# Kernel optimization log

Hardware: AMD Instinct MI355X
Metric: run time of the kernel (lower is better)

## Reference

```python
import jax, jax.numpy as jnp
import numpy as np

CH_IN = 256
CA = CH_IN // 8   # attention channels (theta/phi)
CH = CH_IN // 2   # value channels (g)


def _maxpool2(t):
    # 2x2 max pool, stride 2: (B,C,H,W) -> (B,C,H//2,W//2)
    b, c, h, w = t.shape
    return t.reshape(b, c, h // 2, 2, w // 2, 2).max(axis=(3, 5))


def setup_inputs() -> dict:
    key = jax.random.key(0)
    ks = jax.random.split(key, 6)
    B, H, W = 16, 64, 64
    x = jax.random.normal(ks[0], (B, CH_IN, H, W), dtype=jnp.float32)
    # 1x1 conv weights stored as (out_ch, in_ch); spectral_norm is a weight
    # reparameterization, so the forward math is a plain conv with these weights.
    s = 0.05
    w_theta = jax.random.normal(ks[1], (CA, CH_IN), dtype=jnp.float32) * s
    w_phi = jax.random.normal(ks[2], (CA, CH_IN), dtype=jnp.float32) * s
    w_g = jax.random.normal(ks[3], (CH, CH_IN), dtype=jnp.float32) * s
    w_o = jax.random.normal(ks[4], (CH_IN, CH), dtype=jnp.float32) * s
    # gamma is initialized to 0 in the module; use a nonzero value so the
    # attention branch contributes to the output.
    gamma = jnp.asarray(0.5, dtype=jnp.float32)
    return {"x": x, "w_theta": w_theta, "w_phi": w_phi, "w_g": w_g,
            "w_o": w_o, "gamma": gamma}


def reference(x, w_theta, w_phi, w_g, w_o, gamma):
    B, C, H, W = x.shape
    # 1x1 convs as channel contractions
    theta = jnp.einsum('oc,bchw->bohw', w_theta, x)            # (B,CA,H,W)
    phi = _maxpool2(jnp.einsum('oc,bchw->bohw', w_phi, x))     # (B,CA,H/2,W/2)
    g = _maxpool2(jnp.einsum('oc,bchw->bohw', w_g, x))         # (B,CH,H/2,W/2)
    N = H * W
    M = N // 4
    theta = theta.reshape(B, CA, N)
    phi = phi.reshape(B, CA, M)
    g = g.reshape(B, CH, M)
    # beta = softmax(theta^T phi) over keys (no scaling, as in original)
    beta = jax.nn.softmax(jnp.einsum('bcn,bcm->bnm', theta, phi), axis=-1)  # (B,N,M)
    o = jnp.einsum('bcm,bnm->bcn', g, beta).reshape(B, CH, H, W)
    o = jnp.einsum('oc,bchw->bohw', w_o, o)                    # (B,C,H,W)
    return gamma * o + x
```

## Files before the change

### kernel.cpp

```cpp
#include <hip/hip_runtime.h>
#include <hip/hip_bf16.h>

#define NB 16
#define CIN 256
#define CA 32
#define CH 128
#define NN 4096
#define MM 1024

typedef __attribute__((ext_vector_type(8))) short s16x8;
typedef __attribute__((ext_vector_type(4))) float f32x4;

static __device__ __forceinline__ unsigned short f2bf(float x) {
  __hip_bfloat16 h = __float2bfloat16(x);
  return __builtin_bit_cast(unsigned short, h);
}
static __device__ __forceinline__ float bf2f(unsigned short u) {
  unsigned int v = ((unsigned int)u) << 16;
  return __builtin_bit_cast(float, v);
}
static __device__ __forceinline__ void gload_lds16(const void* g, void* s) {
  __builtin_amdgcn_global_load_lds(
      (const __attribute__((address_space(1))) unsigned int*)g,
      (__attribute__((address_space(3))) unsigned int*)s, 16, 0, 0);
}

__global__ __launch_bounds__(256) void k_wcvt(const float* __restrict__ w_theta,
                                              const float* __restrict__ w_phi,
                                              const float* __restrict__ w_g,
                                              const float* __restrict__ w_o,
                                              unsigned short* __restrict__ wcat2,
                                              unsigned short* __restrict__ wo2) {
  const int i = blockIdx.x * 256 + threadIdx.x;
  if (i < 49152) {
    const int row = i >> 8, c = i & 255;
    const float v = (row < 32) ? w_theta[i]
                  : (row < 64) ? w_phi[i - 8192]
                               : w_g[i - 16384];
    const int dst = ((row >> 4) * 8 + (c >> 5)) * 512 +
                    (((c >> 3) & 3) * 16 + (row & 15)) * 8 + (c & 7);
    wcat2[dst] = f2bf(v);
  } else {
    const int w = i - 49152;
    const int c_out = w >> 7, k = w & 127;
    const int dst = (((c_out >> 4) * 16) + ((k >> 5) * 4) + ((k >> 3) & 3)) * 128 +
                    ((c_out & 15) << 3) + (k & 7);
    wo2[dst] = f2bf(w_o[w]);
  }
}

__global__ __launch_bounds__(512) void k_proj(const float* __restrict__ x,
                                              const unsigned short* __restrict__ wcat2,
                                              unsigned short* __restrict__ theta,
                                              unsigned short* __restrict__ phi2,
                                              unsigned short* __restrict__ g2) {
  __shared__ unsigned short xl[32][140];
  __shared__ unsigned short ol[192][136];
  const int b = blockIdx.y;
  const int t = blockIdx.x;
  const int tid = threadIdx.x;
  const int wv = tid >> 6;
  const int l = tid & 63;
  const int grp = l >> 4, col = l & 15;
  const float* xb = x + (size_t)b * CIN * NN;
  f32x4 acc[12];
#pragma unroll
  for (int r = 0; r < 12; ++r) acc[r] = f32x4{0.f, 0.f, 0.f, 0.f};
#pragma unroll 1
  for (int kc = 0; kc < 8; ++kc) {
#pragma unroll
    for (int s = 0; s < 2; ++s) {
      const int i = tid + s * 512;
      const int cl = i >> 5, nq = i & 31;
      const float4 v = *reinterpret_cast<const float4*>(
          xb + (size_t)(kc * 32 + cl) * NN + t * 128 + nq * 4);
      const unsigned int lo = (unsigned)f2bf(v.x) | ((unsigned)f2bf(v.y) << 16);
      const unsigned int hi = (unsigned)f2bf(v.z) | ((unsigned)f2bf(v.w) << 16);
      *reinterpret_cast<uint2*>(&xl[cl][nq * 4]) = make_uint2(lo, hi);
    }
    __syncthreads();
    s16x8 bfrag;
#pragma unroll
    for (int j = 0; j < 8; ++j)
      bfrag[j] = (short)xl[grp * 8 + j][wv * 16 + col];
#pragma unroll
    for (int r = 0; r < 12; ++r) {
      const s16x8 af = *reinterpret_cast<const s16x8*>(
          wcat2 + (size_t)(r * 8 + kc) * 512 + l * 8);
      acc[r] = __builtin_amdgcn_mfma_f32_16x16x32_bf16(af, bfrag, acc[r], 0, 0, 0);
    }
    __syncthreads();
  }
#pragma unroll
  for (int r = 0; r < 12; ++r)
#pragma unroll
    for (int q = 0; q < 4; ++q)
      ol[r * 16 + grp * 4 + q][wv * 16 + col] = f2bf(acc[r][q]);
  __syncthreads();
  unsigned short* thb = theta + (size_t)b * NN * CA;
  for (int i = tid; i < 128 * 16; i += 512) {
    const int n = i >> 4, cp = (i & 15) << 1;
    const unsigned int v = (unsigned)ol[cp][n] | ((unsigned)ol[cp + 1][n] << 16);
    *reinterpret_cast<unsigned int*>(thb + (size_t)(t * 128 + n) * CA + cp) = v;
  }
  unsigned short* phb2 = phi2 + (size_t)b * MM * CA;
  for (int i = tid; i < 32 * 32; i += 512) {
    const int ca = i & 31, mx = i >> 5;
    const float v = fmaxf(
        fmaxf(bf2f(ol[32 + ca][2 * mx]), bf2f(ol[32 + ca][2 * mx + 1])),
        fmaxf(bf2f(ol[32 + ca][64 + 2 * mx]), bf2f(ol[32 + ca][64 + 2 * mx + 1])));
    const int m = t * 32 + mx;
    phb2[(m >> 4) * 512 + (ca >> 3) * 128 + (m & 15) * 8 + (ca & 7)] = f2bf(v);
  }
  unsigned short* gb2 = g2 + (size_t)b * CH * MM;
  for (int i = tid; i < 128 * 32; i += 512) {
    const int mx = i & 31, c = i >> 5;
    const float v = fmaxf(
        fmaxf(bf2f(ol[64 + c][2 * mx]), bf2f(ol[64 + c][2 * mx + 1])),
        fmaxf(bf2f(ol[64 + c][64 + 2 * mx]), bf2f(ol[64 + c][64 + 2 * mx + 1])));
    gb2[(size_t)(t * 8 + (c >> 4)) * 512 + ((mx >> 3) & 3) * 128 + (c & 15) * 8 +
        (mx & 7)] = f2bf(v);
  }
}

__global__ __launch_bounds__(256, 3) void k_attn_out(
    const unsigned short* __restrict__ theta, const unsigned short* __restrict__ phi2,
    const unsigned short* __restrict__ g2, const unsigned short* __restrict__ wo2,
    const float* __restrict__ x, const float* __restrict__ gammap,
    float* __restrict__ out) {
  __shared__ __align__(16) unsigned short kv[2][10240];
  __shared__ __align__(16) unsigned short pl[4][16][72];
  const int b = blockIdx.y;
  const int tid = threadIdx.x;
  const int wv = tid >> 6;
  const int l = tid & 63;
  const int grp = l >> 4, col = l & 15;
  const int n0 = blockIdx.x * 128 + wv * 32;
  const unsigned short* thb = theta + (size_t)b * NN * CA;
  const unsigned short* ph2b = phi2 + (size_t)b * MM * CA;
  const unsigned short* gb2 = g2 + (size_t)b * CH * MM;
  const s16x8 qf0 = *reinterpret_cast<const s16x8*>(thb + (size_t)(n0 + col) * CA + grp * 8);
  const s16x8 qf1 = *reinterpret_cast<const s16x8*>(thb + (size_t)(n0 + 16 + col) * CA + grp * 8);

  auto STAGE = [&](int buf, int tile) {
    const int mc = tile * 64;
    const unsigned short* ksrc = ph2b + (mc >> 4) * 512;
    const unsigned short* vsrc = gb2 + (size_t)(mc >> 5) * 4096;
#pragma unroll
    for (int q = 0; q < 5; ++q) {
      const int i = wv * 5 + q;
      const unsigned short* src = (i < 4) ? (ksrc + i * 512) : (vsrc + (i - 4) * 512);
      gload_lds16(src + (size_t)l * 8, &kv[buf][i * 512]);
    }
  };

  f32x4 oa0[8], oa1[8];
#pragma unroll
  for (int t = 0; t < 8; ++t) {
    oa0[t] = f32x4{0.f, 0.f, 0.f, 0.f};
    oa1[t] = f32x4{0.f, 0.f, 0.f, 0.f};
  }
  float m0 = -INFINITY, l0 = 0.f, m1 = -INFINITY, l1 = 0.f;
  const f32x4 z4 = {0.f, 0.f, 0.f, 0.f};

  STAGE(0, 0);
  __syncthreads();
#pragma unroll 1
  for (int it = 0; it < 16; ++it) {
    const int cur = it & 1;
    if (it < 15) STAGE(cur ^ 1, it + 1);
    const unsigned short* kb = &kv[cur][0];
    const unsigned short* vb = &kv[cur][2048];
    const int fo = grp * 128 + col * 8;
    const s16x8 kf0 = *reinterpret_cast<const s16x8*>(kb + 0 * 512 + fo);
    const s16x8 kf1 = *reinterpret_cast<const s16x8*>(kb + 1 * 512 + fo);
    const s16x8 kf2 = *reinterpret_cast<const s16x8*>(kb + 2 * 512 + fo);
    const s16x8 kf3 = *reinterpret_cast<const s16x8*>(kb + 3 * 512 + fo);
    f32x4 s00 = __builtin_amdgcn_mfma_f32_16x16x32_bf16(kf0, qf0, z4, 0, 0, 0);
    f32x4 s01 = __builtin_amdgcn_mfma_f32_16x16x32_bf16(kf1, qf0, z4, 0, 0, 0);
    f32x4 s02 = __builtin_amdgcn_mfma_f32_16x16x32_bf16(kf2, qf0, z4, 0, 0, 0);
    f32x4 s03 = __builtin_amdgcn_mfma_f32_16x16x32_bf16(kf3, qf0, z4, 0, 0, 0);
    f32x4 s10 = __builtin_amdgcn_mfma_f32_16x16x32_bf16(kf0, qf1, z4, 0, 0, 0);
    f32x4 s11 = __builtin_amdgcn_mfma_f32_16x16x32_bf16(kf1, qf1, z4, 0, 0, 0);
    f32x4 s12 = __builtin_amdgcn_mfma_f32_16x16x32_bf16(kf2, qf1, z4, 0, 0, 0);
    f32x4 s13 = __builtin_amdgcn_mfma_f32_16x16x32_bf16(kf3, qf1, z4, 0, 0, 0);
    float cm0 = -INFINITY, cm1 = -INFINITY;
#pragma unroll
    for (int r = 0; r < 4; ++r) {
      cm0 = fmaxf(cm0, fmaxf(fmaxf(s00[r], s01[r]), fmaxf(s02[r], s03[r])));
      cm1 = fmaxf(cm1, fmaxf(fmaxf(s10[r], s11[r]), fmaxf(s12[r], s13[r])));
    }
    cm0 = fmaxf(cm0, __shfl_xor(cm0, 16));
    cm0 = fmaxf(cm0, __shfl_xor(cm0, 32));
    cm1 = fmaxf(cm1, __shfl_xor(cm1, 16));
    cm1 = fmaxf(cm1, __shfl_xor(cm1, 32));
    if (!__all(cm0 <= m0 + 8.f && cm1 <= m1 + 8.f)) {
      const float mn0 = fmaxf(m0, cm0), mn1 = fmaxf(m1, cm1);
      const float sc0 = __expf(m0 - mn0), sc1 = __expf(m1 - mn1);
      l0 *= sc0;
      l1 *= sc1;
#pragma unroll
      for (int t = 0; t < 8; ++t) {
#pragma unroll
        for (int r = 0; r < 4; ++r) {
          oa0[t][r] *= sc0;
          oa1[t][r] *= sc1;
        }
      }
      m0 = mn0;
      m1 = mn1;
    }
    s16x8 pfA0, pfB0, pfA1, pfB1;
    {
      float p0[4], p1[4], p2[4], p3[4];
      float cs = 0.f;
#pragma unroll
      for (int r = 0; r < 4; ++r) {
        p0[r] = __expf(s00[r] - m0);
        p1[r] = __expf(s01[r] - m0);
        p2[r] = __expf(s02[r] - m0);
        p3[r] = __expf(s03[r] - m0);
        cs += (p0[r] + p1[r]) + (p2[r] + p3[r]);
      }
      cs += __shfl_xor(cs, 16);
      cs += __shfl_xor(cs, 32);
      l0 += cs;
      *reinterpret_cast<uint2*>(&pl[wv][col][grp * 4]) =
          make_uint2((unsigned)f2bf(p0[0]) | ((unsigned)f2bf(p0[1]) << 16),
                     (unsigned)f2bf(p0[2]) | ((unsigned)f2bf(p0[3]) << 16));
      *reinterpret_cast<uint2*>(&pl[wv][col][16 + grp * 4]) =
          make_uint2((unsigned)f2bf(p1[0]) | ((unsigned)f2bf(p1[1]) << 16),
                     (unsigned)f2bf(p1[2]) | ((unsigned)f2bf(p1[3]) << 16));
      *reinterpret_cast<uint2*>(&pl[wv][col][32 + grp * 4]) =
          make_uint2((unsigned)f2bf(p2[0]) | ((unsigned)f2bf(p2[1]) << 16),
                     (unsigned)f2bf(p2[2]) | ((unsigned)f2bf(p2[3]) << 16));
      *reinterpret_cast<uint2*>(&pl[wv][col][48 + grp * 4]) =
          make_uint2((unsigned)f2bf(p3[0]) | ((unsigned)f2bf(p3[1]) << 16),
                     (unsigned)f2bf(p3[2]) | ((unsigned)f2bf(p3[3]) << 16));
      pfA0 = *reinterpret_cast<const s16x8*>(&pl[wv][col][grp * 8]);
      pfB0 = *reinterpret_cast<const s16x8*>(&pl[wv][col][32 + grp * 8]);
    }
    {
      float p0[4], p1[4], p2[4], p3[4];
      float cs = 0.f;
#pragma unroll
      for (int r = 0; r < 4; ++r) {
        p0[r] = __expf(s10[r] - m1);
        p1[r] = __expf(s11[r] - m1);
        p2[r] = __expf(s12[r] - m1);
        p3[r] = __expf(s13[r] - m1);
        cs += (p0[r] + p1[r]) + (p2[r] + p3[r]);
      }
      cs += __shfl_xor(cs, 16);
      cs += __shfl_xor(cs, 32);
      l1 += cs;
      *reinterpret_cast<uint2*>(&pl[wv][col][grp * 4]) =
          make_uint2((unsigned)f2bf(p0[0]) | ((unsigned)f2bf(p0[1]) << 16),
                     (unsigned)f2bf(p0[2]) | ((unsigned)f2bf(p0[3]) << 16));
      *reinterpret_cast<uint2*>(&pl[wv][col][16 + grp * 4]) =
          make_uint2((unsigned)f2bf(p1[0]) | ((unsigned)f2bf(p1[1]) << 16),
                     (unsigned)f2bf(p1[2]) | ((unsigned)f2bf(p1[3]) << 16));
      *reinterpret_cast<uint2*>(&pl[wv][col][32 + grp * 4]) =
          make_uint2((unsigned)f2bf(p2[0]) | ((unsigned)f2bf(p2[1]) << 16),
                     (unsigned)f2bf(p2[2]) | ((unsigned)f2bf(p2[3]) << 16));
      *reinterpret_cast<uint2*>(&pl[wv][col][48 + grp * 4]) =
          make_uint2((unsigned)f2bf(p3[0]) | ((unsigned)f2bf(p3[1]) << 16),
                     (unsigned)f2bf(p3[2]) | ((unsigned)f2bf(p3[3]) << 16));
      pfA1 = *reinterpret_cast<const s16x8*>(&pl[wv][col][grp * 8]);
      pfB1 = *reinterpret_cast<const s16x8*>(&pl[wv][col][32 + grp * 8]);
    }
#pragma unroll
    for (int t = 0; t < 8; ++t) {
      const s16x8 vfA = *reinterpret_cast<const s16x8*>(vb + t * 512 + fo);
      const s16x8 vfB = *reinterpret_cast<const s16x8*>(vb + 4096 + t * 512 + fo);
      oa0[t] = __builtin_amdgcn_mfma_f32_16x16x32_bf16(vfA, pfA0, oa0[t], 0, 0, 0);
      oa0[t] = __builtin_amdgcn_mfma_f32_16x16x32_bf16(vfB, pfB0, oa0[t], 0, 0, 0);
      oa1[t] = __builtin_amdgcn_mfma_f32_16x16x32_bf16(vfA, pfA1, oa1[t], 0, 0, 0);
      oa1[t] = __builtin_amdgcn_mfma_f32_16x16x32_bf16(vfB, pfB1, oa1[t], 0, 0, 0);
    }
    __syncthreads();
  }
  unsigned short* obw = &kv[0][0] + (size_t)wv * (32 * 136);
  const float ri0 = 1.f / l0, ri1 = 1.f / l1;
#pragma unroll
  for (int t = 0; t < 8; ++t) {
    *reinterpret_cast<uint2*>(obw + col * 136 + t * 16 + grp * 4) =
        make_uint2((unsigned)f2bf(oa0[t][0] * ri0) | ((unsigned)f2bf(oa0[t][1] * ri0) << 16),
                   (unsigned)f2bf(oa0[t][2] * ri0) | ((unsigned)f2bf(oa0[t][3] * ri0) << 16));
    *reinterpret_cast<uint2*>(obw + (16 + col) * 136 + t * 16 + grp * 4) =
        make_uint2((unsigned)f2bf(oa1[t][0] * ri1) | ((unsigned)f2bf(oa1[t][1] * ri1) << 16),
                   (unsigned)f2bf(oa1[t][2] * ri1) | ((unsigned)f2bf(oa1[t][3] * ri1) << 16));
  }
  s16x8 of0[4], of1[4];
#pragma unroll
  for (int ks = 0; ks < 4; ++ks) {
    of0[ks] = *reinterpret_cast<const s16x8*>(obw + col * 136 + ks * 32 + grp * 8);
    of1[ks] = *reinterpret_cast<const s16x8*>(obw + (16 + col) * 136 + ks * 32 + grp * 8);
  }
  const float gamma = gammap[0];
  const float* xb2 = x + (size_t)b * CIN * NN;
  float* outb = out + (size_t)b * CIN * NN;
#pragma unroll 1
  for (int t2 = 0; t2 < 16; ++t2) {
    f32x4 a20 = {0.f, 0.f, 0.f, 0.f};
    f32x4 a21 = {0.f, 0.f, 0.f, 0.f};
#pragma unroll
    for (int ks = 0; ks < 4; ++ks) {
      const s16x8 wf = *reinterpret_cast<const s16x8*>(
          wo2 + (size_t)(t2 * 16 + ks * 4 + grp) * 128 + col * 8);
      a20 = __builtin_amdgcn_mfma_f32_16x16x32_bf16(wf, of0[ks], a20, 0, 0, 0);
      a21 = __builtin_amdgcn_mfma_f32_16x16x32_bf16(wf, of1[ks], a21, 0, 0, 0);
    }
#pragma unroll
    for (int r = 0; r < 4; ++r) {
      const size_t idx = (size_t)(t2 * 16 + grp * 4 + r) * NN + n0 + col;
      outb[idx] = fmaf(gamma, a20[r], xb2[idx]);
      outb[idx + 16] = fmaf(gamma, a21[r], xb2[idx + 16]);
    }
  }
}

extern "C" void kernel_launch(void* const* d_in, const int* in_sizes, int n_in,
                              void* d_out, int out_size, void* d_ws, size_t ws_size,
                              hipStream_t stream) {
  const float* x = (const float*)d_in[0];
  const float* w_theta = (const float*)d_in[1];
  const float* w_phi = (const float*)d_in[2];
  const float* w_g = (const float*)d_in[3];
  const float* w_o = (const float*)d_in[4];
  const float* gamma = (const float*)d_in[5];
  float* out = (float*)d_out;
  char* ws = (char*)d_ws;
  unsigned short* theta = (unsigned short*)(ws + 0);
  unsigned short* phi2 = (unsigned short*)(ws + 4194304);
  unsigned short* g2 = (unsigned short*)(ws + 5242880);
  unsigned short* wo2 = (unsigned short*)(ws + 9437184);
  unsigned short* wcat2 = (unsigned short*)(ws + 9502720);

  k_wcvt<<<dim3(320), 256, 0, stream>>>(w_theta, w_phi, w_g, w_o, wcat2, wo2);
  k_proj<<<dim3(NN / 128, NB), 512, 0, stream>>>(x, wcat2, theta, phi2, g2);
  k_attn_out<<<dim3(NN / 128, NB), 256, 0, stream>>>(theta, phi2, g2, wo2, x, gamma, out);
}
```

Measured before the change: 88.90 us.

## Split attention keys across two wave groups per block and merge softmax states

Doubles the attention kernel block to 512 threads. Two halves of the block each process half of the key range (512 keys) in 32-key tiles with their own double-buffered LDS staging. At the end they merge the online-softmax max/sum statistics and the partial outputs through shared memory, then split the output projection rows between the halves. The aim is more wavefronts in flight per block, which helps hide latency with the same grid size. The cost is extra synchronisation and the merge step, smaller MFMA batches per iteration, and an extra bf16 rounding of the partial sums.

```diff
diff --git a/kernel.cpp b/kernel.cpp
--- a/kernel.cpp
+++ b/kernel.cpp
@@ -123,19 +123,22 @@
   }
 }
 
-__global__ __launch_bounds__(256, 3) void k_attn_out(
+__global__ __launch_bounds__(512, 4) void k_attn_out(
     const unsigned short* __restrict__ theta, const unsigned short* __restrict__ phi2,
     const unsigned short* __restrict__ g2, const unsigned short* __restrict__ wo2,
     const float* __restrict__ x, const float* __restrict__ gammap,
     float* __restrict__ out) {
-  __shared__ __align__(16) unsigned short kv[2][10240];
-  __shared__ __align__(16) unsigned short pl[4][16][72];
+  __shared__ __align__(16) unsigned short kv[2][2][5120];
+  __shared__ __align__(16) unsigned short pl[8][16][40];
+  __shared__ float mlb[8][2][32];
   const int b = blockIdx.y;
   const int tid = threadIdx.x;
   const int wv = tid >> 6;
+  const int h = wv >> 2;
+  const int gw = wv & 3;
   const int l = tid & 63;
   const int grp = l >> 4, col = l & 15;
-  const int n0 = blockIdx.x * 128 + wv * 32;
+  const int n0 = blockIdx.x * 128 + gw * 32;
   const unsigned short* thb = theta + (size_t)b * NN * CA;
   const unsigned short* ph2b = phi2 + (size_t)b * MM * CA;
   const unsigned short* gb2 = g2 + (size_t)b * CH * MM;
@@ -143,14 +146,19 @@
   const s16x8 qf1 = *reinterpret_cast<const s16x8*>(thb + (size_t)(n0 + 16 + col) * CA + grp * 8);
 
   auto STAGE = [&](int buf, int tile) {
-    const int mc = tile * 64;
+    const int mc = h * 512 + tile * 32;
     const unsigned short* ksrc = ph2b + (mc >> 4) * 512;
     const unsigned short* vsrc = gb2 + (size_t)(mc >> 5) * 4096;
-#pragma unroll
-    for (int q = 0; q < 5; ++q) {
-      const int i = wv * 5 + q;
-      const unsigned short* src = (i < 4) ? (ksrc + i * 512) : (vsrc + (i - 4) * 512);
-      gload_lds16(src + (size_t)l * 8, &kv[buf][i * 512]);
+    unsigned short* dst = &kv[h][buf][0];
+#pragma unroll
+    for (int q = 0; q < 2; ++q) {
+      const int i = gw + q * 4;
+      const unsigned short* src = (i < 2) ? (ksrc + i * 512) : (vsrc + (size_t)(i - 2) * 512);
+      gload_lds16(src + (size_t)l * 8, dst + i * 512);
+    }
+    if (gw < 2) {
+      const int i = gw + 8;
+      gload_lds16(vsrc + (size_t)(i - 2) * 512 + (size_t)l * 8, dst + i * 512);
     }
   };
 
@@ -169,26 +177,20 @@
   for (int it = 0; it < 16; ++it) {
     const int cur = it & 1;
     if (it < 15) STAGE(cur ^ 1, it + 1);
-    const unsigned short* kb = &kv[cur][0];
-    const unsigned short* vb = &kv[cur][2048];
+    const unsigned short* kb = &kv[h][cur][0];
+    const unsigned short* vb = kb + 1024;
     const int fo = grp * 128 + col * 8;
-    const s16x8 kf0 = *reinterpret_cast<const s16x8*>(kb + 0 * 512 + fo);
-    const s16x8 kf1 = *reinterpret_cast<const s16x8*>(kb + 1 * 512 + fo);
-    const s16x8 kf2 = *reinterpret_cast<const s16x8*>(kb + 2 * 512 + fo);
-    const s16x8 kf3 = *reinterpret_cast<const s16x8*>(kb + 3 * 512 + fo);
+    const s16x8 kf0 = *reinterpret_cast<const s16x8*>(kb + fo);
+    const s16x8 kf1 = *reinterpret_cast<const s16x8*>(kb + 512 + fo);
     f32x4 s00 = __builtin_amdgcn_mfma_f32_16x16x32_bf16(kf0, qf0, z4, 0, 0, 0);
     f32x4 s01 = __builtin_amdgcn_mfma_f32_16x16x32_bf16(kf1, qf0, z4, 0, 0, 0);
-    f32x4 s02 = __builtin_amdgcn_mfma_f32_16x16x32_bf16(kf2, qf0, z4, 0, 0, 0);
-    f32x4 s03 = __builtin_amdgcn_mfma_f32_16x16x32_bf16(kf3, qf0, z4, 0, 0, 0);
     f32x4 s10 = __builtin_amdgcn_mfma_f32_16x16x32_bf16(kf0, qf1, z4, 0, 0, 0);
     f32x4 s11 = __builtin_amdgcn_mfma_f32_16x16x32_bf16(kf1, qf1, z4, 0, 0, 0);
-    f32x4 s12 = __builtin_amdgcn_mfma_f32_16x16x32_bf16(kf2, qf1, z4, 0, 0, 0);
-    f32x4 s13 = __builtin_amdgcn_mfma_f32_16x16x32_bf16(kf3, qf1, z4, 0, 0, 0);
     float cm0 = -INFINITY, cm1 = -INFINITY;
 #pragma unroll
     for (int r = 0; r < 4; ++r) {
-      cm0 = fmaxf(cm0, fmaxf(fmaxf(s00[r], s01[r]), fmaxf(s02[r], s03[r])));
-      cm1 = fmaxf(cm1, fmaxf(fmaxf(s10[r], s11[r]), fmaxf(s12[r], s13[r])));
+      cm0 = fmaxf(cm0, fmaxf(s00[r], s01[r]));
+      cm1 = fmaxf(cm1, fmaxf(s10[r], s11[r]));
     }
     cm0 = fmaxf(cm0, __shfl_xor(cm0, 16));
     cm0 = fmaxf(cm0, __shfl_xor(cm0, 32));
@@ -210,17 +212,15 @@
       m0 = mn0;
       m1 = mn1;
     }
-    s16x8 pfA0, pfB0, pfA1, pfB1;
+    s16x8 pfA0, pfA1;
     {
-      float p0[4], p1[4], p2[4], p3[4];
+      float p0[4], p1[4];
       float cs = 0.f;
 #pragma unroll
       for (int r = 0; r < 4; ++r) {
         p0[r] = __expf(s00[r] - m0);
         p1[r] = __expf(s01[r] - m0);
-        p2[r] = __expf(s02[r] - m0);
-        p3[r] = __expf(s03[r] - m0);
-        cs += (p0[r] + p1[r]) + (p2[r] + p3[r]);
+        cs += p0[r] + p1[r];
       }
       cs += __shfl_xor(cs, 16);
       cs += __shfl_xor(cs, 32);
@@ -231,25 +231,16 @@
       *reinterpret_cast<uint2*>(&pl[wv][col][16 + grp * 4]) =
           make_uint2((unsigned)f2bf(p1[0]) | ((unsigned)f2bf(p1[1]) << 16),
                      (unsigned)f2bf(p1[2]) | ((unsigned)f2bf(p1[3]) << 16));
-      *reinterpret_cast<uint2*>(&pl[wv][col][32 + grp * 4]) =
-          make_uint2((unsigned)f2bf(p2[0]) | ((unsigned)f2bf(p2[1]) << 16),
-                     (unsigned)f2bf(p2[2]) | ((unsigned)f2bf(p2[3]) << 16));
-      *reinterpret_cast<uint2*>(&pl[wv][col][48 + grp * 4]) =
-          make_uint2((unsigned)f2bf(p3[0]) | ((unsigned)f2bf(p3[1]) << 16),
-                     (unsigned)f2bf(p3[2]) | ((unsigned)f2bf(p3[3]) << 16));
       pfA0 = *reinterpret_cast<const s16x8*>(&pl[wv][col][grp * 8]);
-      pfB0 = *reinterpret_cast<const s16x8*>(&pl[wv][col][32 + grp * 8]);
     }
     {
-      float p0[4], p1[4], p2[4], p3[4];
+      float p0[4], p1[4];
       float cs = 0.f;
 #pragma unroll
       for (int r = 0; r < 4; ++r) {
         p0[r] = __expf(s10[r] - m1);
         p1[r] = __expf(s11[r] - m1);
-        p2[r] = __expf(s12[r] - m1);
-        p3[r] = __expf(s13[r] - m1);
-        cs += (p0[r] + p1[r]) + (p2[r] + p3[r]);
+        cs += p0[r] + p1[r];
       }
       cs += __shfl_xor(cs, 16);
       cs += __shfl_xor(cs, 32);
@@ -260,48 +251,75 @@
       *reinterpret_cast<uint2*>(&pl[wv][col][16 + grp * 4]) =
           make_uint2((unsigned)f2bf(p1[0]) | ((unsigned)f2bf(p1[1]) << 16),
                      (unsigned)f2bf(p1[2]) | ((unsigned)f2bf(p1[3]) << 16));
-      *reinterpret_cast<uint2*>(&pl[wv][col][32 + grp * 4]) =
-          make_uint2((unsigned)f2bf(p2[0]) | ((unsigned)f2bf(p2[1]) << 16),
-                     (unsigned)f2bf(p2[2]) | ((unsigned)f2bf(p2[3]) << 16));
-      *reinterpret_cast<uint2*>(&pl[wv][col][48 + grp * 4]) =
-          make_uint2((unsigned)f2bf(p3[0]) | ((unsigned)f2bf(p3[1]) << 16),
-                     (unsigned)f2bf(p3[2]) | ((unsigned)f2bf(p3[3]) << 16));
       pfA1 = *reinterpret_cast<const s16x8*>(&pl[wv][col][grp * 8]);
-      pfB1 = *reinterpret_cast<const s16x8*>(&pl[wv][col][32 + grp * 8]);
     }
 #pragma unroll
     for (int t = 0; t < 8; ++t) {
       const s16x8 vfA = *reinterpret_cast<const s16x8*>(vb + t * 512 + fo);
-      const s16x8 vfB = *reinterpret_cast<const s16x8*>(vb + 4096 + t * 512 + fo);
       oa0[t] = __builtin_amdgcn_mfma_f32_16x16x32_bf16(vfA, pfA0, oa0[t], 0, 0, 0);
-      oa0[t] = __builtin_amdgcn_mfma_f32_16x16x32_bf16(vfB, pfB0, oa0[t], 0, 0, 0);
       oa1[t] = __builtin_amdgcn_mfma_f32_16x16x32_bf16(vfA, pfA1, oa1[t], 0, 0, 0);
-      oa1[t] = __builtin_amdgcn_mfma_f32_16x16x32_bf16(vfB, pfB1, oa1[t], 0, 0, 0);
     }
     __syncthreads();
   }
-  unsigned short* obw = &kv[0][0] + (size_t)wv * (32 * 136);
-  const float ri0 = 1.f / l0, ri1 = 1.f / l1;
-#pragma unroll
-  for (int t = 0; t < 8; ++t) {
-    *reinterpret_cast<uint2*>(obw + col * 136 + t * 16 + grp * 4) =
-        make_uint2((unsigned)f2bf(oa0[t][0] * ri0) | ((unsigned)f2bf(oa0[t][1] * ri0) << 16),
-                   (unsigned)f2bf(oa0[t][2] * ri0) | ((unsigned)f2bf(oa0[t][3] * ri0) << 16));
-    *reinterpret_cast<uint2*>(obw + (16 + col) * 136 + t * 16 + grp * 4) =
-        make_uint2((unsigned)f2bf(oa1[t][0] * ri1) | ((unsigned)f2bf(oa1[t][1] * ri1) << 16),
-                   (unsigned)f2bf(oa1[t][2] * ri1) | ((unsigned)f2bf(oa1[t][3] * ri1) << 16));
-  }
+  if (grp == 0) {
+    mlb[wv][0][col] = m0;
+    mlb[wv][1][col] = l0;
+    mlb[wv][0][16 + col] = m1;
+    mlb[wv][1][16 + col] = l1;
+  }
+  __syncthreads();
+  const int pw = wv ^ 4;
+  const float mo0 = mlb[pw][0][col], lo0 = mlb[pw][1][col];
+  const float mo1 = mlb[pw][0][16 + col], lo1 = mlb[pw][1][16 + col];
+  const float mt0 = fmaxf(m0, mo0), mt1 = fmaxf(m1, mo1);
+  const float sc0 = __expf(m0 - mt0), sc1 = __expf(m1 - mt1);
+  const float lt0 = l0 * sc0 + lo0 * __expf(mo0 - mt0);
+  const float lt1 = l1 * sc1 + lo1 * __expf(mo1 - mt1);
+  unsigned short* mb = &kv[0][0][0] + (size_t)gw * (32 * 136);
+  if (h == 1) {
+#pragma unroll
+    for (int t = 0; t < 8; ++t) {
+      *reinterpret_cast<uint2*>(mb + col * 136 + t * 16 + grp * 4) =
+          make_uint2((unsigned)f2bf(oa0[t][0] * sc0) | ((unsigned)f2bf(oa0[t][1] * sc0) << 16),
+                     (unsigned)f2bf(oa0[t][2] * sc0) | ((unsigned)f2bf(oa0[t][3] * sc0) << 16));
+      *reinterpret_cast<uint2*>(mb + (16 + col) * 136 + t * 16 + grp * 4) =
+          make_uint2((unsigned)f2bf(oa1[t][0] * sc1) | ((unsigned)f2bf(oa1[t][1] * sc1) << 16),
+                     (unsigned)f2bf(oa1[t][2] * sc1) | ((unsigned)f2bf(oa1[t][3] * sc1) << 16));
+    }
+  }
+  __syncthreads();
+  if (h == 0) {
+    const float ri0 = 1.f / lt0, ri1 = 1.f / lt1;
+#pragma unroll
+    for (int t = 0; t < 8; ++t) {
+      float v0[4], v1[4];
+#pragma unroll
+      for (int q = 0; q < 4; ++q) {
+        v0[q] = (oa0[t][q] * sc0 + bf2f(mb[col * 136 + t * 16 + grp * 4 + q])) * ri0;
+        v1[q] = (oa1[t][q] * sc1 + bf2f(mb[(16 + col) * 136 + t * 16 + grp * 4 + q])) * ri1;
+      }
+      *reinterpret_cast<uint2*>(mb + col * 136 + t * 16 + grp * 4) =
+          make_uint2((unsigned)f2bf(v0[0]) | ((unsigned)f2bf(v0[1]) << 16),
+                     (unsigned)f2bf(v0[2]) | ((unsigned)f2bf(v0[3]) << 16));
+      *reinterpret_cast<uint2*>(mb + (16 + col) * 136 + t * 16 + grp * 4) =
+          make_uint2((unsigned)f2bf(v1[0]) | ((unsigned)f2bf(v1[1]) << 16),
+                     (unsigned)f2bf(v1[2]) | ((unsigned)f2bf(v1[3]) << 16));
+    }
+  }
+  __syncthreads();
   s16x8 of0[4], of1[4];
 #pragma unroll
   for (int ks = 0; ks < 4; ++ks) {
-    of0[ks] = *reinterpret_cast<const s16x8*>(obw + col * 136 + ks * 32 + grp * 8);
-    of1[ks] = *reinterpret_cast<const s16x8*>(obw + (16 + col) * 136 + ks * 32 + grp * 8);
+    of0[ks] = *reinterpret_cast<const s16x8*>(mb + col * 136 + ks * 32 + grp * 8);
+    of1[ks] = *reinterpret_cast<const s16x8*>(mb + (16 + col) * 136 + ks * 32 + grp * 8);
   }
   const float gamma = gammap[0];
   const float* xb2 = x + (size_t)b * CIN * NN;
   float* outb = out + (size_t)b * CIN * NN;
+  const int t2base = h * 8;
 #pragma unroll 1
-  for (int t2 = 0; t2 < 16; ++t2) {
+  for (int t2i = 0; t2i < 8; ++t2i) {
+    const int t2 = t2base + t2i;
     f32x4 a20 = {0.f, 0.f, 0.f, 0.f};
     f32x4 a21 = {0.f, 0.f, 0.f, 0.f};
 #pragma unroll
@@ -339,5 +357,5 @@
 
   k_wcvt<<<dim3(320), 256, 0, stream>>>(w_theta, w_phi, w_g, w_o, wcat2, wo2);
   k_proj<<<dim3(NN / 128, NB), 512, 0, stream>>>(x, wcat2, theta, phi2, g2);
-  k_attn_out<<<dim3(NN / 128, NB), 256, 0, stream>>>(theta, phi2, g2, wo2, x, gamma, out);
-}
+  k_attn_out<<<dim3(NN / 128, NB), 512, 0, stream>>>(theta, phi2, g2, wo2, x, gamma, out);
+}
```

New measurement: 88.23 us. No clear change (-0.8%).

## Restructure attention loop sync, share running max, defer row-sum reductions

Applied to the files above, without the earlier changes.

Replaces the per-iteration __syncthreads with explicit s_barrier pairs and a manual vmcnt wait so the next tile's global-to-LDS prefetch overlaps compute. It merges the two per-query-block running maxima into one shared maximum, moves the exp to exp2 with a prescaled max, and defers the cross-lane row-sum shuffles until after the loop. It also raises wave priority around the PV MFMA block. Sharing one max across both query halves lowers the number of rescales, but it risks precision loss when row maxima differ widely. The hand-written waitcnt depends on the exact count of outstanding loads.

```diff
diff --git a/kernel.cpp b/kernel.cpp
--- a/kernel.cpp
+++ b/kernel.cpp
@@ -149,7 +149,7 @@
 #pragma unroll
     for (int q = 0; q < 5; ++q) {
       const int i = wv * 5 + q;
-      const unsigned short* src = (i < 4) ? (ksrc + i * 512) : (vsrc + (i - 4) * 512);
+      const unsigned short* src = (i < 4) ? (ksrc + i * 512) : (vsrc + (size_t)(i - 4) * 512);
       gload_lds16(src + (size_t)l * 8, &kv[buf][i * 512]);
     }
   };
@@ -160,15 +160,28 @@
     oa0[t] = f32x4{0.f, 0.f, 0.f, 0.f};
     oa1[t] = f32x4{0.f, 0.f, 0.f, 0.f};
   }
-  float m0 = -INFINITY, l0 = 0.f, m1 = -INFINITY, l1 = 0.f;
+  const float L2E = 1.442695041f;
+  float m0 = -INFINITY, mL = -INFINITY;
+  float ls0 = 0.f, ls1 = 0.f;
   const f32x4 z4 = {0.f, 0.f, 0.f, 0.f};
 
   STAGE(0, 0);
-  __syncthreads();
 #pragma unroll 1
   for (int it = 0; it < 16; ++it) {
     const int cur = it & 1;
-    if (it < 15) STAGE(cur ^ 1, it + 1);
+    __builtin_amdgcn_sched_barrier(0);
+    __builtin_amdgcn_s_barrier();
+    __builtin_amdgcn_sched_barrier(0);
+    if (it < 15) {
+      STAGE(cur ^ 1, it + 1);
+      asm volatile("s_waitcnt vmcnt(5)" ::: "memory");
+    } else {
+      asm volatile("s_waitcnt vmcnt(0)" ::: "memory");
+    }
+    __builtin_amdgcn_sched_barrier(0);
+    __builtin_amdgcn_s_barrier();
+    __builtin_amdgcn_sched_barrier(0);
+
     const unsigned short* kb = &kv[cur][0];
     const unsigned short* vb = &kv[cur][2048];
     const int fo = grp * 128 + col * 8;
@@ -184,31 +197,29 @@
     f32x4 s11 = __builtin_amdgcn_mfma_f32_16x16x32_bf16(kf1, qf1, z4, 0, 0, 0);
     f32x4 s12 = __builtin_amdgcn_mfma_f32_16x16x32_bf16(kf2, qf1, z4, 0, 0, 0);
     f32x4 s13 = __builtin_amdgcn_mfma_f32_16x16x32_bf16(kf3, qf1, z4, 0, 0, 0);
-    float cm0 = -INFINITY, cm1 = -INFINITY;
+    float cm = -INFINITY;
 #pragma unroll
     for (int r = 0; r < 4; ++r) {
-      cm0 = fmaxf(cm0, fmaxf(fmaxf(s00[r], s01[r]), fmaxf(s02[r], s03[r])));
-      cm1 = fmaxf(cm1, fmaxf(fmaxf(s10[r], s11[r]), fmaxf(s12[r], s13[r])));
-    }
-    cm0 = fmaxf(cm0, __shfl_xor(cm0, 16));
-    cm0 = fmaxf(cm0, __shfl_xor(cm0, 32));
-    cm1 = fmaxf(cm1, __shfl_xor(cm1, 16));
-    cm1 = fmaxf(cm1, __shfl_xor(cm1, 32));
-    if (!__all(cm0 <= m0 + 8.f && cm1 <= m1 + 8.f)) {
-      const float mn0 = fmaxf(m0, cm0), mn1 = fmaxf(m1, cm1);
-      const float sc0 = __expf(m0 - mn0), sc1 = __expf(m1 - mn1);
-      l0 *= sc0;
-      l1 *= sc1;
+      cm = fmaxf(cm, fmaxf(fmaxf(s00[r], s01[r]), fmaxf(s02[r], s03[r])));
+      cm = fmaxf(cm, fmaxf(fmaxf(s10[r], s11[r]), fmaxf(s12[r], s13[r])));
+    }
+    cm = fmaxf(cm, __shfl_xor(cm, 16));
+    cm = fmaxf(cm, __shfl_xor(cm, 32));
+    if (!__all(cm <= m0 + 8.f)) {
+      const float mn = fmaxf(m0, cm);
+      const float sc = __expf(m0 - mn);
+      ls0 *= sc;
+      ls1 *= sc;
 #pragma unroll
       for (int t = 0; t < 8; ++t) {
 #pragma unroll
         for (int r = 0; r < 4; ++r) {
-          oa0[t][r] *= sc0;
-          oa1[t][r] *= sc1;
+          oa0[t][r] *= sc;
+          oa1[t][r] *= sc;
         }
       }
-      m0 = mn0;
-      m1 = mn1;
+      m0 = mn;
+      mL = m0 * L2E;
     }
     s16x8 pfA0, pfB0, pfA1, pfB1;
     {
@@ -216,15 +227,13 @@
       float cs = 0.f;
 #pragma unroll
       for (int r = 0; r < 4; ++r) {
-        p0[r] = __expf(s00[r] - m0);
-        p1[r] = __expf(s01[r] - m0);
-        p2[r] = __expf(s02[r] - m0);
-        p3[r] = __expf(s03[r] - m0);
+        p0[r] = exp2f(fmaf(s00[r], L2E, -mL));
+        p1[r] = exp2f(fmaf(s01[r], L2E, -mL));
+        p2[r] = exp2f(fmaf(s02[r], L2E, -mL));
+        p3[r] = exp2f(fmaf(s03[r], L2E, -mL));
         cs += (p0[r] + p1[r]) + (p2[r] + p3[r]);
       }
-      cs += __shfl_xor(cs, 16);
-      cs += __shfl_xor(cs, 32);
-      l0 += cs;
+      ls0 += cs;
       *reinterpret_cast<uint2*>(&pl[wv][col][grp * 4]) =
           make_uint2((unsigned)f2bf(p0[0]) | ((unsigned)f2bf(p0[1]) << 16),
                      (unsigned)f2bf(p0[2]) | ((unsigned)f2bf(p0[3]) << 16));
@@ -245,15 +254,13 @@
       float cs = 0.f;
 #pragma unroll
       for (int r = 0; r < 4; ++r) {
-        p0[r] = __expf(s10[r] - m1);
-        p1[r] = __expf(s11[r] - m1);
-        p2[r] = __expf(s12[r] - m1);
-        p3[r] = __expf(s13[r] - m1);
+        p0[r] = exp2f(fmaf(s10[r], L2E, -mL));
+        p1[r] = exp2f(fmaf(s11[r], L2E, -mL));
+        p2[r] = exp2f(fmaf(s12[r], L2E, -mL));
+        p3[r] = exp2f(fmaf(s13[r], L2E, -mL));
         cs += (p0[r] + p1[r]) + (p2[r] + p3[r]);
       }
-      cs += __shfl_xor(cs, 16);
-      cs += __shfl_xor(cs, 32);
-      l1 += cs;
+      ls1 += cs;
       *reinterpret_cast<uint2*>(&pl[wv][col][grp * 4]) =
           make_uint2((unsigned)f2bf(p0[0]) | ((unsigned)f2bf(p0[1]) << 16),
                      (unsigned)f2bf(p0[2]) | ((unsigned)f2bf(p0[3]) << 16));
@@ -269,6 +276,7 @@
       pfA1 = *reinterpret_cast<const s16x8*>(&pl[wv][col][grp * 8]);
       pfB1 = *reinterpret_cast<const s16x8*>(&pl[wv][col][32 + grp * 8]);
     }
+    __builtin_amdgcn_s_setprio(1);
 #pragma unroll
     for (int t = 0; t < 8; ++t) {
       const s16x8 vfA = *reinterpret_cast<const s16x8*>(vb + t * 512 + fo);
@@ -278,10 +286,15 @@
       oa1[t] = __builtin_amdgcn_mfma_f32_16x16x32_bf16(vfA, pfA1, oa1[t], 0, 0, 0);
       oa1[t] = __builtin_amdgcn_mfma_f32_16x16x32_bf16(vfB, pfB1, oa1[t], 0, 0, 0);
     }
-    __syncthreads();
-  }
+    __builtin_amdgcn_s_setprio(0);
+  }
+  __syncthreads();
+  ls0 += __shfl_xor(ls0, 16);
+  ls0 += __shfl_xor(ls0, 32);
+  ls1 += __shfl_xor(ls1, 16);
+  ls1 += __shfl_xor(ls1, 32);
   unsigned short* obw = &kv[0][0] + (size_t)wv * (32 * 136);
-  const float ri0 = 1.f / l0, ri1 = 1.f / l1;
+  const float ri0 = 1.f / ls0, ri1 = 1.f / ls1;
 #pragma unroll
   for (int t = 0; t < 8; ++t) {
     *reinterpret_cast<uint2*>(obw + col * 136 + t * 16 + grp * 4) =
```

Measured after the change: 93.28 us. +4.9%, slower.
